# Optimization experiments

Measured on AMD Instinct MI355X. Metric: run time of the kernel, lower is better.

Reference implementation:

```python
import jax, jax.numpy as jnp
import numpy as np

N_NODES = 50000
D = 128            # input_dim == hidden_dim == output_dim
N_EDGES = 800000   # 2 relation types concatenated
BN_EPS = 1e-5


def _gcn_conv(x, W, b, src, dst, n):
    # PyG GCNConv: add self loops, symmetric normalization, gather-scatter aggregate.
    h = x @ W                                   # [N, D]
    loop = jnp.arange(n)
    s = jnp.concatenate([src, loop])
    d = jnp.concatenate([dst, loop])
    deg = jax.ops.segment_sum(jnp.ones_like(s, dtype=h.dtype), d, num_segments=n)
    dinv = jnp.where(deg > 0, jax.lax.rsqrt(deg), 0.0)
    norm = dinv[s] * dinv[d]                    # [E+N]
    agg = jax.ops.segment_sum(h[s] * norm[:, None], d, num_segments=n)  # [N, D]
    return agg + b


def _batch_norm(x, gamma, beta):
    # BatchNorm1d training-mode math (biased variance over node axis)
    m = x.mean(axis=0)
    v = x.var(axis=0)
    return (x - m) * jax.lax.rsqrt(v + BN_EPS) * gamma + beta


def _gcn_layer(x, src, dst, W, b, gamma, beta, n):
    h = _gcn_conv(x, W, b, src, dst, n)
    h = jax.nn.relu(_batch_norm(h, gamma, beta))
    return h + x  # residual (in_features == out_features); dropout = identity (eval)


def setup_inputs() -> dict:
    key = jax.random.key(0)
    ks = jax.random.split(key, 8)
    x = jax.random.normal(ks[0], (N_NODES, D), dtype=jnp.float32)
    edge_index = jax.random.randint(ks[1], (2, N_EDGES), 0, N_NODES, dtype=jnp.int64)
    sc = 1.0 / np.sqrt(D)
    return {
        "x": x,
        "edge_index": edge_index,
        "W1": jax.random.normal(ks[2], (D, D), dtype=jnp.float32) * sc,
        "b1": jnp.zeros((D,), dtype=jnp.float32),
        "g1": jnp.ones((D,), dtype=jnp.float32),
        "be1": jnp.zeros((D,), dtype=jnp.float32),
        "W2": jax.random.normal(ks[3], (D, D), dtype=jnp.float32) * sc,
        "b2": jnp.zeros((D,), dtype=jnp.float32),
        "g2": jnp.ones((D,), dtype=jnp.float32),
        "be2": jnp.zeros((D,), dtype=jnp.float32),
        "Wa": jax.random.normal(ks[4], (D, 1), dtype=jnp.float32) * sc,
        "ba": jnp.zeros((1,), dtype=jnp.float32),
    }


def reference(x, edge_index, W1, b1, g1, be1, W2, b2, g2, be2, Wa, ba):
    n = x.shape[0]
    src, dst = edge_index[0], edge_index[1]
    h = _gcn_layer(x, src, dst, W1, b1, g1, be1, n)
    h = _gcn_layer(h, src, dst, W2, b2, g2, be2, n)
    att = jax.nn.softmax(jnp.tanh(h @ Wa + ba), axis=0)  # softmax over nodes
    return h * att
```

## Files before the change

### kernel.cpp

```cpp
#include <hip/hip_runtime.h>
#include <hip/hip_fp16.h>

#define NN 50000
#define DD 128
#define NE 800000
#define BN_EPS 1e-5f
#define NBUCK 196
#define TILE_A 4096

typedef _Float16 f16x8 __attribute__((ext_vector_type(8)));
typedef float f32x4 __attribute__((ext_vector_type(4)));

__global__ __launch_bounds__(256) void k_binA1(const int* __restrict__ dst,
                                               int* __restrict__ bucketCnt, int ne) {
    __shared__ int hcnt[NBUCK];
    int tid = threadIdx.x;
    for (int i = tid; i < NBUCK; i += 256) hcnt[i] = 0;
    __syncthreads();
    int base = blockIdx.x * TILE_A;
    int lim = ne - base;
    if (lim > TILE_A) lim = TILE_A;
    for (int i = tid; i < lim; i += 256) atomicAdd(&hcnt[dst[base + i] >> 8], 1);
    __syncthreads();
    for (int b = tid; b < NBUCK; b += 256)
        if (hcnt[b]) atomicAdd(&bucketCnt[b], hcnt[b]);
}

__global__ __launch_bounds__(256) void k_binA2(const int* __restrict__ src,
                                               const int* __restrict__ dst,
                                               const int* __restrict__ bucketCnt,
                                               int* __restrict__ bucketRes,
                                               unsigned* __restrict__ evS, int ne) {
    __shared__ int sc[256];
    __shared__ int sExcl[256];
    __shared__ int hcnt[NBUCK];
    __shared__ int hbase[NBUCK];
    int tid = threadIdx.x;
    int v = (tid < NBUCK) ? bucketCnt[tid] : 0;
    sc[tid] = v;
    __syncthreads();
    for (int off = 1; off < 256; off <<= 1) {
        int add = (tid >= off) ? sc[tid - off] : 0;
        __syncthreads();
        sc[tid] += add;
        __syncthreads();
    }
    sExcl[tid] = sc[tid] - v;
    for (int i = tid; i < NBUCK; i += 256) hcnt[i] = 0;
    __syncthreads();

    int base = blockIdx.x * TILE_A;
    int lim = ne - base;
    if (lim > TILE_A) lim = TILE_A;
    for (int i = tid; i < lim; i += 256) atomicAdd(&hcnt[dst[base + i] >> 8], 1);
    __syncthreads();
    for (int b = tid; b < NBUCK; b += 256) {
        hbase[b] = hcnt[b] ? (sExcl[b] + atomicAdd(&bucketRes[b], hcnt[b])) : 0;
        hcnt[b] = 0;
    }
    __syncthreads();
    for (int i = tid; i < lim; i += 256) {
        int d = dst[base + i];
        int s = src[base + i];
        int bk = d >> 8;
        int rank = atomicAdd(&hcnt[bk], 1);
        evS[hbase[bk] + rank] = (unsigned)s | ((unsigned)(d & 255) << 16);
    }
}

__global__ __launch_bounds__(256) void k_binB(const unsigned* __restrict__ evS,
                                              const int* __restrict__ bucketCnt,
                                              unsigned* __restrict__ ev,
                                              int* __restrict__ rowp,
                                              float* __restrict__ dinv, int n) {
    __shared__ int sc[256];
    __shared__ int ncnt[256];
    __shared__ int nbase[256];
    __shared__ int ncur[256];
    int tid = threadIdx.x;
    int b = blockIdx.x;

    int v = (tid < NBUCK) ? bucketCnt[tid] : 0;
    sc[tid] = v;
    __syncthreads();
    for (int off = 1; off < 256; off <<= 1) {
        int add = (tid >= off) ? sc[tid - off] : 0;
        __syncthreads();
        sc[tid] += add;
        __syncthreads();
    }
    int lo = sc[b] - ((b < NBUCK) ? bucketCnt[b] : 0);
    int cnt_b = bucketCnt[b];

    ncnt[tid] = 0;
    __syncthreads();
    for (int p = tid; p < cnt_b; p += 256)
        atomicAdd(&ncnt[evS[lo + p] >> 16], 1);
    __syncthreads();
    int nv = ncnt[tid];
    sc[tid] = nv;
    __syncthreads();
    for (int off = 1; off < 256; off <<= 1) {
        int add = (tid >= off) ? sc[tid - off] : 0;
        __syncthreads();
        sc[tid] += add;
        __syncthreads();
    }
    nbase[tid] = sc[tid] - nv;
    ncur[tid] = sc[tid] - nv;
    int node0 = b << 8;
    int node = node0 + tid;
    if (node < n) {
        rowp[node] = lo + nbase[tid];
        dinv[node] = 1.0f / sqrtf((float)(nv + 1));
    }
    if (b == NBUCK - 1 && tid == 0) rowp[n] = lo + cnt_b;
    __syncthreads();
    for (int p = tid; p < cnt_b; p += 256) {
        unsigned r = evS[lo + p];
        int ln = r >> 16;
        int rank = atomicAdd(&ncur[ln], 1);
        ev[lo + rank] = r & 0xFFFFu;
    }
}

#define GTILE 64
__global__ __launch_bounds__(256) void k_gemm(const float* __restrict__ A,
                                              const float* __restrict__ res,
                                              const float* __restrict__ sums,
                                              const float* __restrict__ gamma,
                                              const float* __restrict__ beta,
                                              float* __restrict__ Hout,
                                              const float* __restrict__ dscale,
                                              const float* __restrict__ W,
                                              __half* __restrict__ C, int n) {
    __shared__ __half sW[DD * DD];
    __shared__ __half sA[GTILE * DD];
    __shared__ float s_scale[DD], s_shift[DD];
    int tid = threadIdx.x;
    int wave = tid >> 6;
    int lane = tid & 63;
    bool fused = (res != nullptr);

    {
        for (int s = tid; s < DD * DD / 8; s += 256) {
            int l = s & 63;
            int ks = (s >> 6) & 3;
            int cb = s >> 8;
            int col = cb * 16 + (l & 15);
            int kbase = ks * 32 + (l >> 4) * 8;
            __align__(16) __half tmp[8];
            #pragma unroll
            for (int j = 0; j < 8; j++)
                tmp[j] = __float2half_rn(W[(kbase + j) * DD + col]);
            *(uint4*)(sW + s * 8) = *(uint4*)tmp;
        }
    }
    if (fused && tid < DD) {
        float ssum = 0.f, qsum = 0.f;
        #pragma unroll
        for (int b = 0; b < 16; b++) {
            ssum += sums[b * 256 + tid];
            qsum += sums[b * 256 + 128 + tid];
        }
        float inv_n = 1.0f / (float)n;
        float mean = ssum * inv_n;
        float var = qsum * inv_n - mean * mean;
        float sc = gamma[tid] * (1.0f / sqrtf(var + BN_EPS));
        s_scale[tid] = sc;
        s_shift[tid] = beta[tid] - mean * sc;
    }

    int ntiles = (n + GTILE - 1) / GTILE;
    for (int t = blockIdx.x; t < ntiles; t += gridDim.x) {
        int row0 = t * GTILE;
        __syncthreads();
        {
            const float4* Av = (const float4*)(A + (size_t)row0 * DD);
            const float4* Rv = (const float4*)(res + (size_t)row0 * DD);
            float4* Hv = (float4*)(Hout + (size_t)row0 * DD);
            for (int i = tid; i < GTILE * DD / 4; i += 256) {
                int r = i >> 5;
                int kq = i & 31;
                bool rowok = (row0 + r < n);
                float4 v = make_float4(0.f, 0.f, 0.f, 0.f);
                if (rowok) v = Av[i];
                if (fused) {
                    float4 rv = make_float4(0.f, 0.f, 0.f, 0.f);
                    if (rowok) rv = Rv[i];
                    int f4 = kq * 4;
                    v.x = fmaxf(v.x * s_scale[f4]     + s_shift[f4],     0.f) + rv.x;
                    v.y = fmaxf(v.y * s_scale[f4 + 1] + s_shift[f4 + 1], 0.f) + rv.y;
                    v.z = fmaxf(v.z * s_scale[f4 + 2] + s_shift[f4 + 2], 0.f) + rv.z;
                    v.w = fmaxf(v.w * s_scale[f4 + 3] + s_shift[f4 + 3], 0.f) + rv.w;
                    if (rowok) Hv[i] = v;
                }
                __half2 p0 = __floats2half2_rn(v.x, v.y);
                __half2 p1 = __floats2half2_rn(v.z, v.w);
                uint2 pk;
                pk.x = *(unsigned*)&p0;
                pk.y = *(unsigned*)&p1;
                int slot = ((r >> 4) * 4 + (kq >> 3)) * 64 +
                           (((kq >> 1) & 3) << 4) + (r & 15);
                int byte = slot * 16 + (kq & 1) * 8;
                byte ^= ((byte >> 9) & 7) << 4;
                *(uint2*)((char*)sA + byte) = pk;
            }
        }
        __syncthreads();

        f32x4 acc[8];
        #pragma unroll
        for (int cb = 0; cb < 8; cb++) acc[cb] = (f32x4)(0.0f);
        f16x8 af[4];
        #pragma unroll
        for (int ks = 0; ks < 4; ks++) {
            int rb = ((wave * 4 + ks) * 64 + lane) * 16;
            rb ^= ((rb >> 9) & 7) << 4;
            af[ks] = *(const f16x8*)((const char*)sA + rb);
        }
        #pragma unroll
        for (int cb = 0; cb < 8; cb++) {
            #pragma unroll
            for (int ks = 0; ks < 4; ks++) {
                f16x8 bf = *(const f16x8*)(sW + ((cb * 4 + ks) * 64 + lane) * 8);
                acc[cb] = __builtin_amdgcn_mfma_f32_16x16x32_f16(af[ks], bf,
                                                                 acc[cb], 0, 0, 0);
            }
        }

        __syncthreads();

        float dv[4];
        #pragma unroll
        for (int rr = 0; rr < 4; rr++) {
            int row = row0 + wave * 16 + (lane >> 4) * 4 + rr;
            dv[rr] = (row < n) ? dscale[row] : 1.f;
        }

        __half* sC = sA + wave * (16 * DD);
        #pragma unroll
        for (int cb = 0; cb < 8; cb++) {
            int col = cb * 16 + (lane & 15);
            #pragma unroll
            for (int rr = 0; rr < 4; rr++) {
                int grow = (lane >> 4) * 4 + rr;
                sC[grow * DD + (col ^ ((grow & 3) << 4))] =
                    __float2half(acc[cb][rr] * dv[rr]);
            }
        }
        __syncthreads();
        #pragma unroll
        for (int i2 = 0; i2 < 4; i2++) {
            int o = (i2 * 64 + lane) * 8;
            int grow = o >> 7;
            int col0 = o & 127;
            int row = row0 + wave * 16 + grow;
            if (row < n) {
                uint4 val = *(uint4*)(sC + grow * DD + (col0 ^ ((grow & 3) << 4)));
                *(uint4*)(C + (size_t)row * DD + col0) = val;
            }
        }
    }
}

#define ACC8(raw) { const __half2* hp_ = (const __half2*)&(raw);               \
    float2 c0_ = __half22float2(hp_[0]); float2 c1_ = __half22float2(hp_[1]);  \
    float2 c2_ = __half22float2(hp_[2]); float2 c3_ = __half22float2(hp_[3]);  \
    a[0] += c0_.x; a[1] += c0_.y; a[2] += c1_.x; a[3] += c1_.y;                \
    a[4] += c2_.x; a[5] += c2_.y; a[6] += c3_.x; a[7] += c3_.y; }

__global__ __launch_bounds__(256) void k_agg(const __half* __restrict__ h,
                                             const int* __restrict__ rowp,
                                             const unsigned* __restrict__ ev,
                                             const float* __restrict__ dinv,
                                             const float* __restrict__ bias,
                                             float* __restrict__ out,
                                             float* __restrict__ sums, int n) {
    int tid = threadIdx.x;
    int grp = tid >> 4;
    int m = tid & 15;
    int node = blockIdx.x * 16 + grp;
    bool activ = node < n;

    int beg = 0, end = 0;
    float di = 0.f;
    if (activ) { beg = rowp[node]; end = rowp[node + 1]; di = dinv[node]; }

    float sf[8] = {0.f, 0.f, 0.f, 0.f, 0.f, 0.f, 0.f, 0.f};
    float bf[8];
    {
        float4 b0 = *(const float4*)(bias + m * 8);
        float4 b1 = *(const float4*)(bias + m * 8 + 4);
        bf[0] = b0.x; bf[1] = b0.y; bf[2] = b0.z; bf[3] = b0.w;
        bf[4] = b1.x; bf[5] = b1.y; bf[6] = b1.z; bf[7] = b1.w;
        if (activ) {
            float4 raw = *(const float4*)(h + (size_t)node * DD + m * 8);
            const __half2* hp = (const __half2*)&raw;
            float2 s0 = __half22float2(hp[0]);
            float2 s1 = __half22float2(hp[1]);
            float2 s2 = __half22float2(hp[2]);
            float2 s3 = __half22float2(hp[3]);
            sf[0] = s0.x; sf[1] = s0.y; sf[2] = s1.x; sf[3] = s1.y;
            sf[4] = s2.x; sf[5] = s2.y; sf[6] = s3.x; sf[7] = s3.y;
        }
    }

    float a[8] = {0.f, 0.f, 0.f, 0.f, 0.f, 0.f, 0.f, 0.f};
    int e = beg;
    int cnt4 = (end - beg) >> 2;
    if (cnt4 > 0) {
        unsigned s0 = ev[e], s1 = ev[e + 1], s2 = ev[e + 2], s3 = ev[e + 3];
        float4 r0 = *(const float4*)(h + (size_t)s0 * DD + m * 8);
        float4 r1 = *(const float4*)(h + (size_t)s1 * DD + m * 8);
        float4 r2 = *(const float4*)(h + (size_t)s2 * DD + m * 8);
        float4 r3 = *(const float4*)(h + (size_t)s3 * DD + m * 8);
        for (int g = 1; g < cnt4; g++) {
            e += 4;
            unsigned t0 = ev[e], t1 = ev[e + 1], t2 = ev[e + 2], t3 = ev[e + 3];
            float4 q0 = *(const float4*)(h + (size_t)t0 * DD + m * 8);
            float4 q1 = *(const float4*)(h + (size_t)t1 * DD + m * 8);
            float4 q2 = *(const float4*)(h + (size_t)t2 * DD + m * 8);
            float4 q3 = *(const float4*)(h + (size_t)t3 * DD + m * 8);
            ACC8(r0); ACC8(r1); ACC8(r2); ACC8(r3);
            r0 = q0; r1 = q1; r2 = q2; r3 = q3;
        }
        ACC8(r0); ACC8(r1); ACC8(r2); ACC8(r3);
        e += 4;
    }
    for (; e < end; e++) {
        unsigned s = ev[e];
        float4 raw = *(const float4*)(h + (size_t)s * DD + m * 8);
        ACC8(raw);
    }

    float o[8];
    #pragma unroll
    for (int j = 0; j < 8; j++) o[j] = di * (a[j] + sf[j]) + bf[j];
    if (activ) {
        float* op = out + (size_t)node * DD + m * 8;
        *(float4*)op = make_float4(o[0], o[1], o[2], o[3]);
        *(float4*)(op + 4) = make_float4(o[4], o[5], o[6], o[7]);
    }

    __shared__ float rs[16][132];
    #pragma unroll
    for (int j = 0; j < 8; j++) rs[grp][m * 8 + j] = activ ? o[j] : 0.f;
    __syncthreads();

    int bank = blockIdx.x & 15;
    if (tid < 128) {
        float s = 0.f;
        #pragma unroll
        for (int r2 = 0; r2 < 16; r2++) s += rs[r2][tid];
        atomicAdd(&sums[bank * 256 + tid], s);
    } else {
        int f = tid - 128;
        float q = 0.f;
        #pragma unroll
        for (int r2 = 0; r2 < 16; r2++) { float v = rs[r2][f]; q += v * v; }
        atomicAdd(&sums[bank * 256 + 128 + f], q);
    }
}

__global__ __launch_bounds__(256) void k_bn(const float* __restrict__ X,
                                            const float* __restrict__ res,
                                            const float* __restrict__ sums,
                                            const float* __restrict__ gamma,
                                            const float* __restrict__ beta,
                                            const float* __restrict__ Wa,
                                            const float* __restrict__ ba,
                                            float* __restrict__ out,
                                            float* __restrict__ evec,
                                            float* __restrict__ Zb, int n) {
    __shared__ float s_scale[128], s_shift[128];
    if (threadIdx.x < 128) {
        int ff = threadIdx.x;
        float ssum = 0.f, qsum = 0.f;
        #pragma unroll
        for (int b = 0; b < 16; b++) {
            ssum += sums[b * 256 + ff];
            qsum += sums[b * 256 + 128 + ff];
        }
        float inv_n = 1.0f / (float)n;
        float mean = ssum * inv_n;
        float var = qsum * inv_n - mean * mean;
        float sc = gamma[ff] * (1.0f / sqrtf(var + BN_EPS));
        s_scale[ff] = sc;
        s_shift[ff] = beta[ff] - mean * sc;
    }
    __syncthreads();
    int idx = blockIdx.x * 256 + threadIdx.x;
    int total = n * (DD / 4);
    int f = (threadIdx.x & 31) * 4;
    float o[4] = {0.f, 0.f, 0.f, 0.f};
    if (idx < total) {
        float4 v = ((const float4*)X)[idx];
        float4 rv = ((const float4*)res)[idx];
        float vi[4] = {v.x, v.y, v.z, v.w};
        float ri[4] = {rv.x, rv.y, rv.z, rv.w};
        #pragma unroll
        for (int j = 0; j < 4; j++) {
            float x = vi[j] * s_scale[f + j] + s_shift[f + j];
            x = fmaxf(x, 0.f);
            o[j] = x + ri[j];
        }
        ((float4*)out)[idx] = make_float4(o[0], o[1], o[2], o[3]);
    }
    if (Wa != nullptr) {
        float t = 0.f;
        if (idx < total) {
            float4 wv = *(const float4*)(Wa + f);
            t = o[0] * wv.x + o[1] * wv.y + o[2] * wv.z + o[3] * wv.w;
        }
        #pragma unroll
        for (int m = 16; m >= 1; m >>= 1) t += __shfl_xor(t, m);
        __shared__ float part[8];
        if ((threadIdx.x & 31) == 0) {
            float ev = 0.f;
            if (idx < total) {
                ev = expf(tanhf(t + ba[0]));
                evec[idx >> 5] = ev;
            }
            part[threadIdx.x >> 5] = ev;
        }
        __syncthreads();
        if (threadIdx.x == 0) {
            float z = part[0] + part[1] + part[2] + part[3] +
                      part[4] + part[5] + part[6] + part[7];
            atomicAdd(&Zb[blockIdx.x & 63], z);
        }
    }
}

__global__ __launch_bounds__(256) void k_out(const float* __restrict__ H,
                                             const float* __restrict__ evec,
                                             const float* __restrict__ Zb,
                                             float* __restrict__ out, int n) {
    __shared__ float sZ;
    if (threadIdx.x == 0) {
        float z = 0.f;
        #pragma unroll
        for (int i = 0; i < 64; i++) z += Zb[i];
        sZ = z;
    }
    __syncthreads();
    int idx = blockIdx.x * blockDim.x + threadIdx.x;
    int total = n * (DD / 4);
    if (idx >= total) return;
    int node = idx >> 5;
    float s = evec[node] / sZ;
    float4 h = ((const float4*)H)[idx];
    ((float4*)out)[idx] = make_float4(h.x * s, h.y * s, h.z * s, h.w * s);
}

extern "C" void kernel_launch(void* const* d_in, const int* in_sizes, int n_in,
                              void* d_out, int out_size, void* d_ws, size_t ws_size,
                              hipStream_t stream) {
    const float* x   = (const float*)d_in[0];
    const int* eidx  = (const int*)d_in[1];
    const float* W1  = (const float*)d_in[2];
    const float* b1  = (const float*)d_in[3];
    const float* g1  = (const float*)d_in[4];
    const float* be1 = (const float*)d_in[5];
    const float* W2  = (const float*)d_in[6];
    const float* b2  = (const float*)d_in[7];
    const float* g2  = (const float*)d_in[8];
    const float* be2 = (const float*)d_in[9];
    const float* Wa  = (const float*)d_in[10];
    const float* ba  = (const float*)d_in[11];
    float* out = (float*)d_out;

    const int* srcp = eidx;
    const int* dstp = eidx + NE;

    float* bufA = (float*)d_ws;
    float* bufB = bufA + (size_t)NN * DD;
    float* bufC = bufB + (size_t)NN * DD;
    unsigned* ev = (unsigned*)(bufC + (size_t)NN * DD);
    float* dinv = (float*)(ev + NE);
    float* evec = dinv + NN;
    int* bucketCnt = (int*)(evec + NN);
    int* bucketRes = bucketCnt + 256;
    float* sums = (float*)(bucketRes + 256);
    float* Zb   = sums + 8192;
    int* rowp   = (int*)(Zb + 64);

    __half* hH  = (__half*)bufA;
    unsigned* evS = (unsigned*)bufB;

    float* sumsL1 = sums;
    float* sumsL2 = sums + 4096;

    hipMemsetAsync(bucketCnt, 0, (size_t)(256 + 256 + 8192 + 64) * sizeof(int),
                   stream);
    const int nA = (NE + TILE_A - 1) / TILE_A;
    k_binA1<<<nA, 256, 0, stream>>>(dstp, bucketCnt, NE);
    k_binA2<<<nA, 256, 0, stream>>>(srcp, dstp, bucketCnt, bucketRes, evS, NE);
    k_binB<<<NBUCK, 256, 0, stream>>>(evS, bucketCnt, ev, rowp, dinv, NN);

    int gemm_grid = (NN + GTILE - 1) / GTILE;
    int agg_grid  = (NN + 15) / 16;
    int ew_grid   = (NN * (DD / 4) + 255) / 256;

    k_gemm<<<gemm_grid, 256, 0, stream>>>(x, nullptr, nullptr, nullptr, nullptr,
                                          nullptr, dinv, W1, hH, NN);
    k_agg<<<agg_grid, 256, 0, stream>>>(hH, rowp, ev, dinv, b1, bufB, sumsL1, NN);

    k_gemm<<<gemm_grid, 256, 0, stream>>>(bufB, x, sumsL1, g1, be1, bufC,
                                          dinv, W2, hH, NN);
    k_agg<<<agg_grid, 256, 0, stream>>>(hH, rowp, ev, dinv, b2, bufB, sumsL2, NN);
    k_bn<<<ew_grid, 256, 0, stream>>>(bufB, bufC, sumsL2, g2, be2, Wa, ba,
                                      bufC, evec, Zb, NN);

    k_out<<<ew_grid, 256, 0, stream>>>(bufC, evec, Zb, out, NN);
}
```

Before: 273.3 us.

## Fuse CSR build memset and three binning kernels into one cooperative kernel

Replaces the memset plus the three CSR-construction kernels (bucket count, bucket scatter, per-node sort) with a single cooperative kernel that uses grid-wide syncs between phases. This relies on the edge-tile count (196 tiles of 4096) equalling the bucket count so one grid covers both phases. It removes three kernel launches and the memset, at the cost of grid barriers and a grid limited to 196 co-resident blocks.

```diff
diff --git a/kernel.cpp b/kernel.cpp
--- a/kernel.cpp
+++ b/kernel.cpp
@@ -1,5 +1,8 @@
 #include <hip/hip_runtime.h>
 #include <hip/hip_fp16.h>
+#include <hip/hip_cooperative_groups.h>
+
+namespace cg = cooperative_groups;
 
 #define NN 50000
 #define DD 128
@@ -11,48 +14,53 @@
 typedef _Float16 f16x8 __attribute__((ext_vector_type(8)));
 typedef float f32x4 __attribute__((ext_vector_type(4)));
 
-__global__ __launch_bounds__(256) void k_binA1(const int* __restrict__ dst,
-                                               int* __restrict__ bucketCnt, int ne) {
-    __shared__ int hcnt[NBUCK];
-    int tid = threadIdx.x;
-    for (int i = tid; i < NBUCK; i += 256) hcnt[i] = 0;
-    __syncthreads();
-    int base = blockIdx.x * TILE_A;
-    int lim = ne - base;
-    if (lim > TILE_A) lim = TILE_A;
-    for (int i = tid; i < lim; i += 256) atomicAdd(&hcnt[dst[base + i] >> 8], 1);
-    __syncthreads();
-    for (int b = tid; b < NBUCK; b += 256)
-        if (hcnt[b]) atomicAdd(&bucketCnt[b], hcnt[b]);
-}
-
-__global__ __launch_bounds__(256) void k_binA2(const int* __restrict__ src,
-                                               const int* __restrict__ dst,
-                                               const int* __restrict__ bucketCnt,
-                                               int* __restrict__ bucketRes,
-                                               unsigned* __restrict__ evS, int ne) {
+__global__ __launch_bounds__(256) void k_csr(const int* __restrict__ src,
+                                             const int* __restrict__ dst,
+                                             int* __restrict__ bucketCnt,
+                                             int* __restrict__ bucketRes,
+                                             unsigned* __restrict__ evS,
+                                             unsigned* __restrict__ ev,
+                                             int* __restrict__ rowp,
+                                             float* __restrict__ dinv,
+                                             int ne, int n) {
+    cg::grid_group grid = cg::this_grid();
     __shared__ int sc[256];
     __shared__ int sExcl[256];
     __shared__ int hcnt[NBUCK];
     __shared__ int hbase[NBUCK];
+    __shared__ int ncnt[256];
+    __shared__ int ncur[256];
     int tid = threadIdx.x;
-    int v = (tid < NBUCK) ? bucketCnt[tid] : 0;
-    sc[tid] = v;
-    __syncthreads();
-    for (int off = 1; off < 256; off <<= 1) {
-        int add = (tid >= off) ? sc[tid - off] : 0;
-        __syncthreads();
-        sc[tid] += add;
-        __syncthreads();
-    }
-    sExcl[tid] = sc[tid] - v;
+    int blk = blockIdx.x;
+
+    for (int i = blk * 256 + tid; i < 8768; i += NBUCK * 256) bucketCnt[i] = 0;
+    __threadfence();
+    grid.sync();
+
     for (int i = tid; i < NBUCK; i += 256) hcnt[i] = 0;
     __syncthreads();
-
-    int base = blockIdx.x * TILE_A;
+    int base = blk * TILE_A;
     int lim = ne - base;
     if (lim > TILE_A) lim = TILE_A;
     for (int i = tid; i < lim; i += 256) atomicAdd(&hcnt[dst[base + i] >> 8], 1);
+    __syncthreads();
+    for (int b = tid; b < NBUCK; b += 256)
+        if (hcnt[b]) atomicAdd(&bucketCnt[b], hcnt[b]);
+    __threadfence();
+    grid.sync();
+
+    {
+        int v = (tid < NBUCK) ? bucketCnt[tid] : 0;
+        sc[tid] = v;
+        __syncthreads();
+        for (int off = 1; off < 256; off <<= 1) {
+            int add = (tid >= off) ? sc[tid - off] : 0;
+            __syncthreads();
+            sc[tid] += add;
+            __syncthreads();
+        }
+        sExcl[tid] = sc[tid] - v;
+    }
     __syncthreads();
     for (int b = tid; b < NBUCK; b += 256) {
         hbase[b] = hcnt[b] ? (sExcl[b] + atomicAdd(&bucketRes[b], hcnt[b])) : 0;
@@ -66,22 +74,18 @@
         int rank = atomicAdd(&hcnt[bk], 1);
         evS[hbase[bk] + rank] = (unsigned)s | ((unsigned)(d & 255) << 16);
     }
-}
-
-__global__ __launch_bounds__(256) void k_binB(const unsigned* __restrict__ evS,
-                                              const int* __restrict__ bucketCnt,
-                                              unsigned* __restrict__ ev,
-                                              int* __restrict__ rowp,
-                                              float* __restrict__ dinv, int n) {
-    __shared__ int sc[256];
-    __shared__ int ncnt[256];
-    __shared__ int nbase[256];
-    __shared__ int ncur[256];
-    int tid = threadIdx.x;
-    int b = blockIdx.x;
-
-    int v = (tid < NBUCK) ? bucketCnt[tid] : 0;
-    sc[tid] = v;
+    __threadfence();
+    grid.sync();
+
+    int lo = sExcl[blk];
+    int cnt_b = bucketCnt[blk];
+    ncnt[tid] = 0;
+    __syncthreads();
+    for (int p = tid; p < cnt_b; p += 256)
+        atomicAdd(&ncnt[evS[lo + p] >> 16], 1);
+    __syncthreads();
+    int nv = ncnt[tid];
+    sc[tid] = nv;
     __syncthreads();
     for (int off = 1; off < 256; off <<= 1) {
         int add = (tid >= off) ? sc[tid - off] : 0;
@@ -89,32 +93,14 @@
         sc[tid] += add;
         __syncthreads();
     }
-    int lo = sc[b] - ((b < NBUCK) ? bucketCnt[b] : 0);
-    int cnt_b = bucketCnt[b];
-
-    ncnt[tid] = 0;
-    __syncthreads();
-    for (int p = tid; p < cnt_b; p += 256)
-        atomicAdd(&ncnt[evS[lo + p] >> 16], 1);
-    __syncthreads();
-    int nv = ncnt[tid];
-    sc[tid] = nv;
-    __syncthreads();
-    for (int off = 1; off < 256; off <<= 1) {
-        int add = (tid >= off) ? sc[tid - off] : 0;
-        __syncthreads();
-        sc[tid] += add;
-        __syncthreads();
-    }
-    nbase[tid] = sc[tid] - nv;
-    ncur[tid] = sc[tid] - nv;
-    int node0 = b << 8;
-    int node = node0 + tid;
+    int nb = sc[tid] - nv;
+    ncur[tid] = nb;
+    int node = (blk << 8) + tid;
     if (node < n) {
-        rowp[node] = lo + nbase[tid];
+        rowp[node] = lo + nb;
         dinv[node] = 1.0f / sqrtf((float)(nv + 1));
     }
-    if (b == NBUCK - 1 && tid == 0) rowp[n] = lo + cnt_b;
+    if (blk == NBUCK - 1 && tid == 0) rowp[n] = lo + cnt_b;
     __syncthreads();
     for (int p = tid; p < cnt_b; p += 256) {
         unsigned r = evS[lo + p];
@@ -492,12 +478,15 @@
     float* sumsL1 = sums;
     float* sumsL2 = sums + 4096;
 
-    hipMemsetAsync(bucketCnt, 0, (size_t)(256 + 256 + 8192 + 64) * sizeof(int),
-                   stream);
-    const int nA = (NE + TILE_A - 1) / TILE_A;
-    k_binA1<<<nA, 256, 0, stream>>>(dstp, bucketCnt, NE);
-    k_binA2<<<nA, 256, 0, stream>>>(srcp, dstp, bucketCnt, bucketRes, evS, NE);
-    k_binB<<<NBUCK, 256, 0, stream>>>(evS, bucketCnt, ev, rowp, dinv, NN);
+    int ne_c = NE, n_c = NN;
+
+    {
+        void* args[] = {(void*)&srcp, (void*)&dstp, (void*)&bucketCnt,
+                        (void*)&bucketRes, (void*)&evS, (void*)&ev,
+                        (void*)&rowp, (void*)&dinv, (void*)&ne_c, (void*)&n_c};
+        hipLaunchCooperativeKernel((const void*)k_csr, dim3(NBUCK), dim3(256),
+                                   args, 0, stream);
+    }
 
     int gemm_grid = (NN + GTILE - 1) / GTILE;
     int agg_grid  = (NN + 15) / 16;
```

Result: slower. 408.3 us (+49.4%).
